# Performance work log

Measured on AMD Instinct MI355X. Metric: run time of the kernel, lower is better.

The kernel has to match this reference:

```python
import jax, jax.numpy as jnp
import numpy as np

PATCH = 8
EPS = 1e-5

def patch_split(x, s):
    # B C H W -> B s*s rH rW C
    B, C, H, W = x.shape
    rH, rW = H // s, W // s
    out = x.reshape(B, C, s, rH, s, rW)
    out = out.transpose(0, 2, 4, 3, 5, 1)
    return out.reshape(B, s * s, rH, rW, C)

def patch_recover(x, s):
    # B s*s rH rW C -> B C H W
    B, N, rH, rW, C = x.shape
    out = x.reshape(B, s, s, rH, rW, C)
    out = out.transpose(0, 5, 1, 3, 2, 4)
    return out.reshape(B, C, s * rH, s * rW)

def conv2d(x, w, pad):
    return jax.lax.conv_general_dilated(x, w, (1, 1), [(pad, pad), (pad, pad)],
                                        dimension_numbers=('NCHW', 'OIHW', 'NCHW'))

def bn_relu(x, g, b):
    # eval-mode BatchNorm2d with fresh running stats (mean=0, var=1)
    scale = (g / jnp.sqrt(1.0 + EPS))[None, :, None, None]
    return jax.nn.relu(x * scale + b[None, :, None, None])


def setup_inputs() -> dict:
    key = jax.random.key(0)
    ks = jax.random.split(key, 24)
    r = lambda i, shape, s=0.02: jax.random.normal(ks[i], shape, jnp.float32) * s
    B, H, W, C, K, P = 4, 64, 64, 512, 19, 64
    return {
        'M_1': jax.random.normal(ks[0], (B, 2048, H, W), jnp.float32),
        'F': jax.random.normal(ks[1], (B, C, H, W), jnp.float32),
        'I': jax.random.normal(ks[2], (B, K, H, W), jnp.float32),
        'R': jax.random.uniform(ks[3], (B, K, PATCH, PATCH), jnp.float32),
        'lg_w1': r(4, (P, P)), 'lg_w2': r(5, (C, C)),
        'fuse_w': r(6, (P,)), 'fuse_b': r(7, (1,)),
        'q_w': r(8, (256, C)), 'q_b': r(9, (256,)),
        'k_w': r(10, (256, C)), 'k_b': r(11, (256,)),
        'v_w': r(12, (256, C)), 'v_b': r(13, (256,)),
        'c1_w': r(14, (512, 256, 1, 1)),
        'bn1_g': jnp.ones((512,)), 'bn1_b': jnp.zeros((512,)),
        'c2_w': r(15, (512, 512, 3, 3)),
        'bn2_g': jnp.ones((512,)), 'bn2_b': jnp.zeros((512,)),
        'c3_w': r(16, (512, 2560, 3, 3)),
        'bn3_g': jnp.ones((512,)), 'bn3_b': jnp.zeros((512,)),
        'drop_w': r(17, (K, 512, 1, 1)),
    }


def reference(M_1, F, I, R, lg_w1, lg_w2, fuse_w, fuse_b, q_w, q_b, k_w, k_b,
              v_w, v_b, c1_w, bn1_g, bn1_b, c2_w, bn2_g, bn2_b, c3_w, bn3_g,
              bn3_b, drop_w):
    B = F.shape[0]
    F_p5 = patch_split(F, PATCH)          # B P rH rW C
    _, P, rH, rW, C = F_p5.shape
    I_p5 = patch_split(I, PATCH)          # B P rH rW K
    K = I_p5.shape[-1]
    F_p = F_p5.reshape(B, P, rH * rW, C)
    I_p = I_p5.reshape(B, P, rH * rW, K)
    bin_conf = R.reshape(B, K, P).transpose(0, 2, 1)[..., None]  # B P K 1
    pix = jax.nn.softmax(I_p, axis=2)
    F_l = jnp.einsum('bpnk,bpnc->bpkc', pix, F_p) * bin_conf     # B P K C
    # LG block: 1x1 conv over P channels, residual relu, linear over C
    h = jnp.einsum('qp,bpkc->bqkc', lg_w1, F_l)
    h = jax.nn.relu(h + F_l)
    F_l = jnp.einsum('bpkc,dc->bpkd', h, lg_w2)
    # FUSE: 1x1 conv P->1 (with bias); broadcast replaces torch .repeat
    F_g = jnp.einsum('p,bpkc->bkc', fuse_w, F_l) + fuse_b        # B K C
    query = jnp.einsum('bpnc,dc->bpnd', F_p, q_w) + q_b          # B P N 256
    key_ = jnp.einsum('bpkc,dc->bpkd', F_l, k_w) + k_b           # B P K 256
    value = jnp.einsum('bkc,dc->bkd', F_g, v_w) + v_b            # B K 256
    aff = jax.nn.softmax(jnp.einsum('bpnd,bpkd->bpnk', query, key_), axis=-1)
    F_s = jnp.einsum('bpnk,bkd->bpnd', aff, value)               # B P N 256
    F_s = patch_recover(F_s.reshape(B, P, rH, rW, -1), PATCH)    # B 256 H W
    Fo1 = F + bn_relu(conv2d(F_s, c1_w, 0), bn1_g, bn1_b)
    x2 = bn_relu(conv2d(Fo1, c2_w, 1), bn2_g, bn2_b)
    x3 = bn_relu(conv2d(jnp.concatenate([x2, M_1], axis=1), c3_w, 1), bn3_g, bn3_b)
    # Dropout2d is identity in eval; final 1x1 classifier conv
    return conv2d(x3, drop_w, 0)
```

## Files before the change

kernel.cpp:

```cpp
#include <hip/hip_runtime.h>
#include <hip/hip_bf16.h>

typedef __hip_bfloat16 bf16;
using short8 = __attribute__((ext_vector_type(8))) short;
using f32x4  = __attribute__((ext_vector_type(4))) float;

__device__ __forceinline__ float b2f(bf16 v){ return __bfloat162float(v); }
__device__ __forceinline__ bf16  f2b(float v){ return __float2bfloat16(v); }

#define EPSV 1e-5f

__device__ __forceinline__ void gload16(const void* g, void* l) {
  __builtin_amdgcn_global_load_lds(
      (const __attribute__((address_space(1))) unsigned int*)g,
      (__attribute__((address_space(3))) unsigned int*)l, 16, 0, 0);
}

__global__ __launch_bounds__(256) void k_cast4(
    const float* __restrict__ a, bf16* __restrict__ ao,
    const float* __restrict__ b, bf16* __restrict__ bo,
    const float* __restrict__ c, bf16* __restrict__ co,
    const float* __restrict__ d, bf16* __restrict__ dd) {
  int i = blockIdx.x * 256 + threadIdx.x;
  const float* src; bf16* dst; int off;
  if (i < 32768)       { src = a; dst = ao; off = i; }
  else if (i < 65536)  { src = b; dst = bo; off = i - 32768; }
  else if (i < 131072) { src = c; dst = co; off = i - 65536; }
  else                 { src = d; dst = dd; off = i - 131072; }
  float4 v = ((const float4*)src)[off];
  union { ushort4 u; bf16 h[4]; } o;
  o.h[0] = f2b(v.x); o.h[1] = f2b(v.y); o.h[2] = f2b(v.z); o.h[3] = f2b(v.w);
  ((ushort4*)dst)[off] = o.u;
}

__global__ __launch_bounds__(256) void k_wtr2(
    const float* __restrict__ wa, bf16* __restrict__ wta,
    const float* __restrict__ wb, bf16* __restrict__ wtb) {
  int oc = blockIdx.x, yy = blockIdx.y;
  const float* w; bf16* wt; int CI, c0;
  if (yy < 4) { w = wa; wt = wta; CI = 512;  c0 = yy * 128; }
  else        { w = wb; wt = wtb; CI = 2560; c0 = (yy - 4) * 128; }
  __shared__ float ld[128 * 9];
  const float* src = w + ((size_t)oc * CI + c0) * 9;
  for (int i = threadIdx.x; i < 128 * 9; i += 256) ld[i] = src[i];
  __syncthreads();
  for (int i = threadIdx.x; i < 128 * 9; i += 256) {
    int k9 = i / 128, t = i - k9 * 128;
    wt[((size_t)k9 * 512 + oc) * CI + c0 + t] = f2b(ld[t * 9 + k9]);
  }
}

__global__ __launch_bounds__(256) void k_m1t(const float* __restrict__ M1,
                                             bf16* __restrict__ M1b) {
  int b = blockIdx.x >> 6, y = blockIdx.x & 63;
  int c0 = blockIdx.y * 64;
  __shared__ float t[64][65];
  for (int i = threadIdx.x; i < 4096; i += 256) {
    int cc = i >> 6, x = i & 63;
    t[x][cc] = M1[((size_t)(b * 2048 + c0 + cc) * 64 + y) * 64 + x];
  }
  __syncthreads();
  for (int i = threadIdx.x; i < 4096; i += 256) {
    int x = i >> 6, cc = i & 63;
    M1b[((size_t)((b * 64 + y) * 64 + x)) * 2048 + c0 + cc] = f2b(t[x][cc]);
  }
}

__global__ __launch_bounds__(256) void k_fp2(const float* __restrict__ F,
                                             bf16* __restrict__ FP) {
  int b = blockIdx.x >> 6, y = blockIdx.x & 63;
  int tid = threadIdx.x;
  __shared__ float t[256][65];
  int p_hi = (y >> 3) << 3, n_hi = (y & 7) << 3;
  for (int half = 0; half < 2; half++) {
    int c0 = half << 8;
    for (int i = tid; i < 256 * 64; i += 256) {
      int cc = i >> 6, x = i & 63;
      t[cc][x] = F[((size_t)(b * 512 + c0 + cc) * 64 + y) * 64 + x];
    }
    __syncthreads();
    for (int x = 0; x < 64; x++) {
      int p = p_hi + (x >> 3), n = n_hi + (x & 7);
      FP[((size_t)(b * 64 + p)) * 32768 + n * 512 + c0 + tid] = f2b(t[tid][x]);
    }
    __syncthreads();
  }
}

__global__ __launch_bounds__(256) void k_flocal2(const float* __restrict__ I,
        const float* __restrict__ R, const bf16* __restrict__ FP,
        float* __restrict__ FL0) {
  int bp = blockIdx.x, b = bp >> 6, p = bp & 63;
  int tid = threadIdx.x, w = tid >> 6, lane = tid & 63;
  __shared__ __align__(16) bf16 fps[64 * 512];
  __shared__ float pix[19][64];
  __shared__ float bc[19];
  {
    const bf16* src = FP + (size_t)bp * 32768 + lane * 8;
    #pragma unroll
    for (int t = 0; t < 16; t++) {
      int chunk = w + t * 4;
      gload16(src + chunk * 512, (char*)fps + chunk * 1024);
    }
  }
  int py = (p >> 3) * 8, px = (p & 7) * 8;
  for (int i = tid; i < 19 * 64; i += 256) {
    int k = i >> 6, n = i & 63;
    int y = py + (n >> 3), x = px + (n & 7);
    pix[k][n] = I[((size_t)(b * 19 + k) * 64 + y) * 64 + x];
  }
  if (tid < 19) bc[tid] = R[(size_t)(b * 19 + tid) * 64 + p];
  __syncthreads();
  if (tid < 19) {
    float mx = -1e30f;
    for (int n = 0; n < 64; n++) mx = fmaxf(mx, pix[tid][n]);
    float s = 0.f;
    for (int n = 0; n < 64; n++) { float e = __expf(pix[tid][n] - mx); pix[tid][n] = e; s += e; }
    float sc = bc[tid] / s;
    for (int n = 0; n < 64; n++) pix[tid][n] *= sc;
  }
  __syncthreads();
  for (int task = tid; task < 19 * 64; task += 256) {
    int k = task >> 6, c8 = (task & 63) << 3;
    float acc[8] = {};
    for (int n = 0; n < 64; n++) {
      float pv = pix[k][n];
      union { short8 s; bf16 h[8]; } v;
      v.s = *(const short8*)&fps[n * 512 + c8];
      #pragma unroll
      for (int j = 0; j < 8; j++) acc[j] += pv * b2f(v.h[j]);
    }
    float* dst = FL0 + ((size_t)(b * 64 + p) * 19 + k) * 512 + c8;
    #pragma unroll
    for (int j = 0; j < 8; j++) dst[j] = acc[j];
  }
}

__global__ __launch_bounds__(256) void k_lg1(const float* __restrict__ FL0,
        const float* __restrict__ w1, bf16* __restrict__ Hb) {
  int tid = threadIdx.x;
  int b = blockIdx.y;
  int n0 = blockIdx.x * 256;
  __shared__ float W[64][64];
  __shared__ float Xs[16][256];
  for (int i = tid; i < 4096; i += 256) W[i >> 6][i & 63] = w1[i];
  float acc[64];
  #pragma unroll
  for (int po = 0; po < 64; po++) acc[po] = 0.f;
  for (int q0 = 0; q0 < 64; q0 += 16) {
    __syncthreads();
    for (int i = tid; i < 4096; i += 256) {
      int q = i >> 8, j = i & 255;
      Xs[q][j] = FL0[(size_t)(b * 64 + q0 + q) * 9728 + n0 + j];
    }
    __syncthreads();
    for (int q = 0; q < 16; q++) {
      float xv = Xs[q][tid];
      #pragma unroll
      for (int po = 0; po < 64; po++) acc[po] += W[po][q0 + q] * xv;
    }
  }
  for (int po = 0; po < 64; po++) {
    float r = acc[po] + FL0[(size_t)(b * 64 + po) * 9728 + n0 + tid];
    Hb[(size_t)(b * 64 + po) * 9728 + n0 + tid] = f2b(fmaxf(r, 0.f));
  }
}

template<int MODE>
__global__ __launch_bounds__(256) void k_gmm(
    const bf16* __restrict__ A, const bf16* __restrict__ B,
    const float* __restrict__ bias, float* __restrict__ C,
    bf16* __restrict__ Cb, int N, int K,
    const float* __restrict__ g, const float* __restrict__ bb,
    const float* __restrict__ Fres, bf16* __restrict__ outb) {
  int tid = threadIdx.x;
  int m0 = blockIdx.x * 128, n0 = blockIdx.y * 128;
  int w = tid >> 6, lane = tid & 63, ln = lane & 15, qd = lane >> 4;
  int wm = w & 1, wn = w >> 1;
  __shared__ __align__(16) char smem[34816];

  f32x4 acc[4][4];
  #pragma unroll
  for (int i = 0; i < 4; i++)
    #pragma unroll
    for (int j = 0; j < 4; j++) acc[i][j] = (f32x4){0.f, 0.f, 0.f, 0.f};

  int rsub = lane >> 2, ch = lane & 3;
  auto stage = [&](int p) {
    char* base = smem + (p & 1) * 16384;
    int k0 = p << 5;
    #pragma unroll
    for (int t = 0; t < 2; t++) {
      int ii = w + t * 4;
      int r = ii * 16 + rsub;
      int sw = (ch ^ ((r >> 1) & 3)) << 3;
      gload16(A + (size_t)(m0 + r) * K + k0 + sw, base + ii * 1024);
      gload16(B + (size_t)(n0 + r) * K + k0 + sw, base + 8192 + ii * 1024);
    }
  };
  auto compute = [&](int p) {
    const char* base = smem + (p & 1) * 16384;
    short8 af[4], bv[4];
    #pragma unroll
    for (int mi = 0; mi < 4; mi++) {
      int r = wm * 64 + mi * 16 + ln;
      af[mi] = *(const short8*)(base + r * 64 + ((qd ^ ((r >> 1) & 3)) << 4));
    }
    #pragma unroll
    for (int ni = 0; ni < 4; ni++) {
      int r = wn * 64 + ni * 16 + ln;
      bv[ni] = *(const short8*)(base + 8192 + r * 64 + ((qd ^ ((r >> 1) & 3)) << 4));
    }
    #pragma unroll
    for (int mi = 0; mi < 4; mi++)
      #pragma unroll
      for (int ni = 0; ni < 4; ni++)
        acc[mi][ni] = __builtin_amdgcn_mfma_f32_16x16x32_bf16(
            af[mi], bv[ni], acc[mi][ni], 0, 0, 0);
  };

  int KT = K >> 5;
  stage(0);
  __syncthreads();
  for (int p = 0; p < KT; p++) {
    if (p + 1 < KT) stage(p + 1);
    compute(p);
    __syncthreads();
  }

  if (MODE <= 1) {
    #pragma unroll
    for (int mi = 0; mi < 4; mi++) {
      #pragma unroll
      for (int r = 0; r < 4; r++) {
        int m = m0 + wm * 64 + mi * 16 + qd * 4 + r;
        #pragma unroll
        for (int ni = 0; ni < 4; ni++) {
          int n = n0 + wn * 64 + ni * 16 + ln;
          float v = acc[mi][ni][r];
          if (bias) v += bias[n];
          C[(size_t)m * N + n] = v;
          if (MODE == 1) Cb[(size_t)m * N + n] = f2b(v);
        }
      }
    }
  } else {
    bf16* EP = (bf16*)smem;
    int b = n0 >> 12;
    #pragma unroll
    for (int mi = 0; mi < 4; mi++) {
      #pragma unroll
      for (int r = 0; r < 4; r++) {
        int ml = wm * 64 + mi * 16 + qd * 4 + r;
        int oc = m0 + ml;
        float sc = g[oc] * rsqrtf(1.f + EPSV);
        float bt = bb[oc];
        #pragma unroll
        for (int ni = 0; ni < 4; ni++) {
          int nl = wn * 64 + ni * 16 + ln;
          int pix = n0 + nl;
          int y = (pix >> 6) & 63, x = pix & 63;
          float v = fmaxf(acc[mi][ni][r] * sc + bt, 0.f)
                  + Fres[((size_t)(b * 512 + oc) * 64 + y) * 64 + x];
          EP[nl * 136 + ml] = f2b(v);
        }
      }
    }
    __syncthreads();
    int pl = tid >> 1, half = tid & 1;
    size_t gb = (size_t)(n0 + pl) * 512 + m0 + half * 64;
    const bf16* row = &EP[pl * 136 + half * 64];
    #pragma unroll
    for (int j2 = 0; j2 < 8; j2++)
      *(short8*)(outb + gb + j2 * 8) = *(const short8*)(row + j2 * 8);
  }
}

__global__ __launch_bounds__(256) void k_fusev(const float* __restrict__ FL,
        const float* __restrict__ fw, const float* __restrict__ fbv,
        const float* __restrict__ vw, const float* __restrict__ vb,
        float* __restrict__ VAL) {
  int tid = threadIdx.x;
  int bk = blockIdx.x, b = bk / 19, k = bk % 19;
  __shared__ float fwl[64];
  __shared__ __align__(16) float fg[512];
  if (tid < 64) fwl[tid] = fw[tid];
  __syncthreads();
  float fbias = fbv[0];
  for (int c = tid; c < 512; c += 256) {
    float s = 0.f;
    for (int p = 0; p < 64; p++)
      s += fwl[p] * FL[((size_t)(b * 64 + p) * 19 + k) * 512 + c];
    fg[c] = s + fbias;
  }
  __syncthreads();
  int d = tid;
  float s = vb[d];
  const float4* vr = (const float4*)(vw + (size_t)d * 512);
  const float4* fr = (const float4*)fg;
  for (int c4 = 0; c4 < 128; c4++) {
    float4 wv = vr[c4], f = fr[c4];
    s += f.x * wv.x + f.y * wv.y + f.z * wv.z + f.w * wv.w;
  }
  VAL[(size_t)bk * 256 + d] = s;
}

__global__ __launch_bounds__(256) void k_attn(const float* __restrict__ Q,
        const float* __restrict__ KEY, const float* __restrict__ VAL,
        bf16* __restrict__ FS) {
  int tid = threadIdx.x;
  int bp = blockIdx.x, b = bp >> 6, p = bp & 63;
  __shared__ __align__(16) float ks[19][256];
  __shared__ __align__(16) float vs[19][256];
  __shared__ float Ss[64][20];
  __shared__ bf16 ot[64][256];
  for (int i = tid; i < 19 * 256; i += 256) {
    ks[i >> 8][i & 255] = KEY[(size_t)bp * 19 * 256 + i];
    vs[i >> 8][i & 255] = VAL[(size_t)b * 19 * 256 + i];
  }
  __syncthreads();
  {
    int n = tid >> 2, kq = tid & 3;
    const float4* qrow = (const float4*)(Q + ((size_t)bp * 64 + n) * 256);
    for (int k = kq; k < 19; k += 4) {
      const float4* kr = (const float4*)&ks[k][0];
      float s = 0.f;
      for (int d4 = 0; d4 < 64; d4++) {
        float4 qv = qrow[d4], kv = kr[d4];
        s += qv.x * kv.x + qv.y * kv.y + qv.z * kv.z + qv.w * kv.w;
      }
      Ss[n][k] = s;
    }
  }
  __syncthreads();
  if (tid < 64) {
    float mx = -1e30f;
    for (int k = 0; k < 19; k++) mx = fmaxf(mx, Ss[tid][k]);
    float sum = 0.f;
    for (int k = 0; k < 19; k++) { float e = __expf(Ss[tid][k] - mx); Ss[tid][k] = e; sum += e; }
    float inv = 1.f / sum;
    for (int k = 0; k < 19; k++) Ss[tid][k] *= inv;
  }
  __syncthreads();
  {
    int d = tid;
    for (int nn = 0; nn < 64; nn++) {
      float s = 0.f;
      #pragma unroll
      for (int k = 0; k < 19; k++) s += Ss[nn][k] * vs[k][d];
      ot[nn][d] = f2b(s);
    }
  }
  __syncthreads();
  {
    int py = (p >> 3) * 8, px = (p & 7) * 8;
    int nn = tid >> 2, q = tid & 3;
    int y = py + (nn >> 3), x = px + (nn & 7);
    size_t gb = (((size_t)(b * 64 + y) * 64) + x) * 256 + q * 64;
    const bf16* row = &ot[nn][q * 64];
    #pragma unroll
    for (int j = 0; j < 8; j++)
      *(short8*)(FS + gb + j * 8) = *(const short8*)(row + j * 8);
  }
}

__global__ __launch_bounds__(512) void k_conv3(
    const bf16* __restrict__ Xin, int Cin,
    const bf16* __restrict__ M1b, const float* __restrict__ M1f, int C2,
    const bf16* __restrict__ WT,
    const float* __restrict__ g, const float* __restrict__ bb,
    bf16* __restrict__ out, int Cos) {
  int tid = threadIdx.x;
  int b = blockIdx.x >> 4, y0 = (blockIdx.x & 15) * 4;
  int oc0 = blockIdx.y * 128;
  int w = tid >> 6, lane = tid & 63, ln = lane & 15, qd = lane >> 4;
  int wocg = w & 1, wyp = w >> 1;
  int Ct = Cin + C2;

  __shared__ __align__(16) char smem[125440];
  char* smA  = smem;
  char* smB  = smem + 73728;
  char* dump = smem + 124416;

  for (int bufi = 0; bufi < 2; bufi++) {
    char* bbuf = smB + bufi * 25344;
    for (int i = tid; i < 6 * 2 * 32; i += 512) {
      int rl = i >> 6, hh = (i >> 5) & 1, kk = i & 31;
      *(bf16*)(bbuf + (rl * 66 + (hh ? 65 : 0)) * 64 + kk * 2) = f2b(0.f);
    }
    if (y0 == 0)
      for (int i = tid; i < 66 * 16; i += 512) ((float*)bbuf)[i] = 0.f;
    if (y0 == 60)
      for (int i = tid; i < 66 * 16; i += 512)
        ((float*)(bbuf + 5 * 66 * 64))[i] = 0.f;
  }

  f32x4 acc[4][4];
  #pragma unroll
  for (int i = 0; i < 4; i++)
    #pragma unroll
    for (int j = 0; j < 4; j++) acc[i][j] = (f32x4){0.f, 0.f, 0.f, 0.f};

  int ngroups = Ct >> 5;
  int NPH = ngroups * 3;

  auto stageA = [&](int p) {
    int c0 = (p / 3) << 5, ky = p % 3;
    char* base = smA + (p % 3 == p - (p / 3) * 3 ? 0 : 0) ;
    base = smA + (p % 3) * 0;
    base = smA + ((p % 3) == 0 ? 0 : 0);
    base = smA + ky * 0;
    base = smA + (p % 3) * 24576;
    #pragma unroll
    for (int t = 0; t < 3; t++) {
      int j = w + t * 8;
      int kx = j >> 3, i8 = j & 7;
      int ocl = i8 * 16 + (lane >> 2);
      const bf16* src = WT + ((size_t)((ky * 3 + kx) * 512 + oc0 + ocl) * Ct + c0)
                      + (((lane & 3) ^ ((ocl >> 1) & 3)) << 3);
      gload16(src, base + (kx * 128 + i8 * 16) * 64);
    }
  };
  auto stageB = [&](int gi) {
    int c0 = gi << 5;
    char* bbuf = smB + (gi & 1) * 25344;
    if (c0 < Cin || M1b != nullptr) {
      const bf16* T; int Cs, cb;
      if (c0 < Cin) { T = Xin; Cs = Cin; cb = c0; }
      else          { T = M1b; Cs = C2;  cb = c0 - Cin; }
      #pragma unroll
      for (int t = 0; t < 3; t++) {
        int j = w + t * 8;
        int rl = j >> 2, q = j & 3;
        int yy = y0 + rl - 1;
        bool ok = (unsigned)yy < 64u;
        int yc = ok ? yy : y0;
        int xx = q * 16 + (lane >> 2), xr = xx + 1;
        const bf16* src = T + ((size_t)((b * 64 + yc) * 64 + xx) * Cs + cb)
                        + (((lane & 3) ^ ((xr >> 1) & 3)) << 3);
        char* dst = ok ? (bbuf + (rl * 66 + 1 + q * 16) * 64) : dump;
        gload16(src, dst);
      }
    } else {
      if (w < 6) {
        int rl = w, yy = y0 + rl - 1;
        if ((unsigned)yy < 64u) {
          int xx = lane, xr = xx + 1;
          const float* mp = M1f + ((size_t)(b * 2048 + (c0 - Cin)) * 64 + yy) * 64 + xx;
          #pragma unroll
          for (int q = 0; q < 8; q++) {
            union { ushort4 u; bf16 h[4]; } pk;
            #pragma unroll
            for (int jj = 0; jj < 4; jj++) pk.h[jj] = f2b(mp[(size_t)(q * 4 + jj) * 4096]);
            *(ushort4*)(bbuf + (rl * 66 + xr) * 64
                        + ((((q >> 1) ^ ((xr >> 1) & 3)) << 4) | ((q & 1) << 3))) = pk.u;
          }
        }
      }
      asm volatile("s_waitcnt lgkmcnt(0)" ::: "memory");
    }
  };
  auto computeP = [&](int p) {
    int ky = p % 3;
    const char* base = smA + (p % 3) * 24576;
    const char* bB   = smB + ((p / 3) & 1) * 25344;
    int rl = wyp + ky;
    #pragma unroll
    for (int kx = 0; kx < 3; kx++) {
      short8 af[4], bv[4];
      #pragma unroll
      for (int mi = 0; mi < 4; mi++) {
        int ocl = wocg * 64 + mi * 16 + ln;
        af[mi] = *(const short8*)(base + (kx * 128 + ocl) * 64
                                  + ((qd ^ ((ocl >> 1) & 3)) << 4));
      }
      #pragma unroll
      for (int ni = 0; ni < 4; ni++) {
        int xr = ni * 16 + ln + kx;
        bv[ni] = *(const short8*)(bB + (rl * 66 + xr) * 64
                                  + ((qd ^ ((xr >> 1) & 3)) << 4));
      }
      #pragma unroll
      for (int mi = 0; mi < 4; mi++)
        #pragma unroll
        for (int ni = 0; ni < 4; ni++)
          acc[mi][ni] = __builtin_amdgcn_mfma_f32_16x16x32_bf16(
              af[mi], bv[ni], acc[mi][ni], 0, 0, 0);
    }
  };

  stageB(0);
  stageA(0);
  stageA(1);
  asm volatile("s_waitcnt lgkmcnt(0)" ::: "memory");

  for (int p = 0; p < NPH; p++) {
    __builtin_amdgcn_s_barrier();
    __builtin_amdgcn_sched_barrier(0);
    if (p + 2 < NPH) stageA(p + 2);
    int pm3 = p % 3;
    int gn = p / 3 + 1;
    bool bValid = gn < ngroups;
    bool bFastN = bValid && (((gn << 5) < Cin) || (M1b != nullptr));
    if (pm3 == 1 && bValid) stageB(gn);
    __builtin_amdgcn_sched_barrier(0);
    int N = (p + 1 < NPH ? 3 : 0) + (p + 2 < NPH ? 3 : 0)
          + ((pm3 != 0 && bFastN) ? 3 : 0);
    if (N == 9)      asm volatile("s_waitcnt vmcnt(9)" ::: "memory");
    else if (N == 6) asm volatile("s_waitcnt vmcnt(6)" ::: "memory");
    else if (N == 3) asm volatile("s_waitcnt vmcnt(3)" ::: "memory");
    else             asm volatile("s_waitcnt vmcnt(0)" ::: "memory");
    __builtin_amdgcn_sched_barrier(0);
    __builtin_amdgcn_s_setprio(1);
    computeP(p);
    __builtin_amdgcn_s_setprio(0);
  }
  __syncthreads();

  {
    bf16* EP = (bf16*)smem;
    #pragma unroll
    for (int mi = 0; mi < 4; mi++) {
      int oclb = wocg * 64 + mi * 16 + qd * 4;
      float sc[4], bt[4];
      #pragma unroll
      for (int r = 0; r < 4; r++) {
        int oc = oc0 + oclb + r;
        sc[r] = g[oc] * rsqrtf(1.f + EPSV);
        bt[r] = bb[oc];
      }
      #pragma unroll
      for (int ni = 0; ni < 4; ni++) {
        int x = ni * 16 + ln;
        union { ushort4 u; bf16 h[4]; } pk;
        #pragma unroll
        for (int r = 0; r < 4; r++)
          pk.h[r] = f2b(fmaxf(acc[mi][ni][r] * sc[r] + bt[r], 0.f));
        *(ushort4*)&EP[(wyp * 64 + x) * 128 + oclb] = pk.u;
      }
    }
    __syncthreads();
    int pixl = tid >> 1, hh = tid & 1;
    int yloc = pixl >> 6, x = pixl & 63;
    size_t gb = ((size_t)((b * 64 + y0 + yloc) * 64 + x)) * Cos + oc0 + hh * 64;
    const bf16* row = &EP[pixl * 128 + hh * 64];
    #pragma unroll
    for (int k = 0; k < 8; k++)
      *(short8*)(out + gb + k * 8) = *(const short8*)(row + k * 8);
  }
}

__global__ __launch_bounds__(256) void k_final(const bf16* __restrict__ X3,
        const float* __restrict__ dw, float* __restrict__ out) {
  int tid = threadIdx.x;
  int b = blockIdx.x >> 6, y = blockIdx.x & 63;
  __shared__ float W[19 * 512];
  for (int i = tid; i < 19 * 512; i += 256) W[i] = dw[i];
  __syncthreads();
  int x = tid & 63, kg = tid >> 6;
  const bf16* px = X3 + (((size_t)(b * 64 + y) * 64) + x) * 512;
  float acc[5] = {0.f, 0.f, 0.f, 0.f, 0.f};
  for (int c8 = 0; c8 < 512; c8 += 8) {
    union { short8 s; bf16 h[8]; } v;
    v.s = *(const short8*)(px + c8);
    float f[8];
    #pragma unroll
    for (int j = 0; j < 8; j++) f[j] = b2f(v.h[j]);
    #pragma unroll
    for (int i = 0; i < 5; i++) {
      int k = kg * 5 + i;
      if (k < 19) {
        const float* wr = &W[k * 512 + c8];
        #pragma unroll
        for (int j = 0; j < 8; j++) acc[i] += f[j] * wr[j];
      }
    }
  }
  for (int i = 0; i < 5; i++) {
    int k = kg * 5 + i;
    if (k < 19) out[((size_t)(b * 19 + k) * 64 + y) * 64 + x] = acc[i];
  }
}

extern "C" void kernel_launch(void* const* d_in, const int* in_sizes, int n_in,
                              void* d_out, int out_size, void* d_ws, size_t ws_size,
                              hipStream_t stream) {
  (void)in_sizes; (void)n_in; (void)out_size;
  const float* M1 = (const float*)d_in[0];
  const float* F  = (const float*)d_in[1];
  const float* Iin= (const float*)d_in[2];
  const float* R  = (const float*)d_in[3];
  const float* w1 = (const float*)d_in[4];
  const float* w2 = (const float*)d_in[5];
  const float* fw = (const float*)d_in[6];
  const float* fb = (const float*)d_in[7];
  const float* qw = (const float*)d_in[8];
  const float* qb = (const float*)d_in[9];
  const float* kw = (const float*)d_in[10];
  const float* kb = (const float*)d_in[11];
  const float* vw = (const float*)d_in[12];
  const float* vb = (const float*)d_in[13];
  const float* c1 = (const float*)d_in[14];
  const float* g1 = (const float*)d_in[15];
  const float* b1 = (const float*)d_in[16];
  const float* c2 = (const float*)d_in[17];
  const float* g2 = (const float*)d_in[18];
  const float* b2 = (const float*)d_in[19];
  const float* c3 = (const float*)d_in[20];
  const float* g3 = (const float*)d_in[21];
  const float* b3 = (const float*)d_in[22];
  const float* dw = (const float*)d_in[23];

  char* ws = (char*)d_ws;
  bool fast = ws_size >= (size_t)137363456ULL;

  bf16*  qwb  = (bf16*)(ws + 0);
  bf16*  kwb  = (bf16*)(ws + 262144);
  bf16*  w2b  = (bf16*)(ws + 524288);
  bf16*  c1b  = (bf16*)(ws + 1048576);
  bf16*  WT2  = (bf16*)(ws + 0);
  bf16*  WT3  = (bf16*)(ws + 4718592);
  bf16*  FS   = (bf16*)(ws + 28311552);
  bf16*  FO1  = (bf16*)(ws + 36700160);
  bf16*  X2   = (bf16*)(ws + 53477376);
  bf16*  M1bf = fast ? (bf16*)(ws + 70254592) : nullptr;
  bf16*  X3   = (bf16*)(ws + 28311552);
  bf16*  FP    = (bf16*) (ws + 53477376);
  float* QUERY = (float*)(ws + 70254592);
  float* FL0   = (float*)(ws + 87031808);
  bf16*  Hb    = (bf16*) (ws + 96993280);
  bf16*  FLb   = (bf16*) (ws + 101974016);
  float* KEY   = (float*)(ws + 106954752);
  float* VAL   = (float*)(ws + 111935488);
  float* FL    = FL0;

  k_cast4<<<640, 256, 0, stream>>>(qw, qwb, kw, kwb, w2, w2b, c1, c1b);
  k_fp2<<<256, 256, 0, stream>>>(F, FP);
  k_flocal2<<<256, 256, 0, stream>>>(Iin, R, FP, FL0);
  k_lg1<<<dim3(38, 4), 256, 0, stream>>>(FL0, w1, Hb);
  k_gmm<1><<<dim3(38, 4), 256, 0, stream>>>(Hb, w2b, nullptr, FL, FLb, 512, 512,
                                            nullptr, nullptr, nullptr, nullptr);
  k_fusev<<<76, 256, 0, stream>>>(FL, fw, fb, vw, vb, VAL);
  k_gmm<0><<<dim3(38, 2), 256, 0, stream>>>(FLb, kwb, kb, KEY, nullptr, 256, 512,
                                            nullptr, nullptr, nullptr, nullptr);
  k_gmm<0><<<dim3(128, 2), 256, 0, stream>>>(FP, qwb, qb, QUERY, nullptr, 256, 512,
                                             nullptr, nullptr, nullptr, nullptr);
  k_attn<<<256, 256, 0, stream>>>(QUERY, KEY, VAL, FS);
  if (fast) k_m1t<<<dim3(256, 32), 256, 0, stream>>>(M1, M1bf);
  k_gmm<2><<<dim3(4, 128), 256, 0, stream>>>(c1b, FS, nullptr, nullptr, nullptr,
                                             16384, 256, g1, b1, F, FO1);
  k_wtr2<<<dim3(512, 24), 256, 0, stream>>>(c2, WT2, c3, WT3);
  k_conv3<<<dim3(64, 4), 512, 0, stream>>>(FO1, 512, nullptr, nullptr, 0,
                                           WT2, g2, b2, X2, 512);
  k_conv3<<<dim3(64, 4), 512, 0, stream>>>(X2, 512, M1bf, M1, 2048,
                                           WT3, g3, b3, X3, 512);
  k_final<<<256, 256, 0, stream>>>(X3, dw, (float*)d_out);
}
```

Baseline: 972.0 us.

## Load conv3 weights directly into registers instead of staging through LDS

Removes the LDS staging buffer for the weight (A) operand of the 3x3 conv over the concatenated input. Each lane now loads its own MFMA A fragments from global memory into registers and double-buffers them across ky phases, while only the input tile (B) stays in shared memory. This cuts LDS use from about 125KB to about 66KB, which could allow more blocks per CU, and drops the LDS traffic for A. In exchange it adds many register-held fragments and uncoalesced 16-byte global loads whose latency is no longer hidden by the explicit vmcnt pipelining, and several waves re-read the same weights from global memory.

```diff
diff --git a/kernel.cpp b/kernel.cpp
--- a/kernel.cpp
+++ b/kernel.cpp
@@ -377,10 +377,9 @@
   int wocg = w & 1, wyp = w >> 1;
   int Ct = Cin + C2;
 
-  __shared__ __align__(16) char smem[125440];
-  char* smA  = smem;
-  char* smB  = smem + 73728;
-  char* dump = smem + 124416;
+  __shared__ __align__(16) char smem[66560];
+  char* smB  = smem;
+  char* dump = smem + 65536;
 
   for (int bufi = 0; bufi < 2; bufi++) {
     char* bbuf = smB + bufi * 25344;
@@ -402,25 +401,9 @@
     for (int j = 0; j < 4; j++) acc[i][j] = (f32x4){0.f, 0.f, 0.f, 0.f};
 
   int ngroups = Ct >> 5;
-  int NPH = ngroups * 3;
-
-  auto stageA = [&](int p) {
-    int c0 = (p / 3) << 5, ky = p % 3;
-    char* base = smA + (p % 3 == p - (p / 3) * 3 ? 0 : 0) ;
-    base = smA + (p % 3) * 0;
-    base = smA + ((p % 3) == 0 ? 0 : 0);
-    base = smA + ky * 0;
-    base = smA + (p % 3) * 24576;
-    #pragma unroll
-    for (int t = 0; t < 3; t++) {
-      int j = w + t * 8;
-      int kx = j >> 3, i8 = j & 7;
-      int ocl = i8 * 16 + (lane >> 2);
-      const bf16* src = WT + ((size_t)((ky * 3 + kx) * 512 + oc0 + ocl) * Ct + c0)
-                      + (((lane & 3) ^ ((ocl >> 1) & 3)) << 3);
-      gload16(src, base + (kx * 128 + i8 * 16) * 64);
-    }
-  };
+
+  const bf16* Alane = WT + (size_t)(oc0 + wocg * 64 + ln) * Ct + qd * 8;
+
   auto stageB = [&](int gi) {
     int c0 = gi << 5;
     char* bbuf = smB + (gi & 1) * 25344;
@@ -457,23 +440,22 @@
           }
         }
       }
-      asm volatile("s_waitcnt lgkmcnt(0)" ::: "memory");
     }
   };
-  auto computeP = [&](int p) {
-    int ky = p % 3;
-    const char* base = smA + (p % 3) * 24576;
-    const char* bB   = smB + ((p / 3) & 1) * 25344;
+  auto loadA = [&](short8* dst, int ky, int c0) {
+    #pragma unroll
+    for (int kx = 0; kx < 3; kx++)
+      #pragma unroll
+      for (int mi = 0; mi < 4; mi++)
+        dst[kx * 4 + mi] = *(const short8*)(Alane
+            + (size_t)((ky * 3 + kx) * 512 + mi * 16) * Ct + c0);
+  };
+  auto computeP = [&](const short8* A, int ky, int gpar) {
+    const char* bB = smB + gpar * 25344;
     int rl = wyp + ky;
     #pragma unroll
     for (int kx = 0; kx < 3; kx++) {
-      short8 af[4], bv[4];
-      #pragma unroll
-      for (int mi = 0; mi < 4; mi++) {
-        int ocl = wocg * 64 + mi * 16 + ln;
-        af[mi] = *(const short8*)(base + (kx * 128 + ocl) * 64
-                                  + ((qd ^ ((ocl >> 1) & 3)) << 4));
-      }
+      short8 bv[4];
       #pragma unroll
       for (int ni = 0; ni < 4; ni++) {
         int xr = ni * 16 + ln + kx;
@@ -485,37 +467,37 @@
         #pragma unroll
         for (int ni = 0; ni < 4; ni++)
           acc[mi][ni] = __builtin_amdgcn_mfma_f32_16x16x32_bf16(
-              af[mi], bv[ni], acc[mi][ni], 0, 0, 0);
+              A[kx * 4 + mi], bv[ni], acc[mi][ni], 0, 0, 0);
     }
   };
 
+  short8 Aa[12], Ab[12];
   stageB(0);
-  stageA(0);
-  stageA(1);
-  asm volatile("s_waitcnt lgkmcnt(0)" ::: "memory");
-
-  for (int p = 0; p < NPH; p++) {
-    __builtin_amdgcn_s_barrier();
-    __builtin_amdgcn_sched_barrier(0);
-    if (p + 2 < NPH) stageA(p + 2);
-    int pm3 = p % 3;
-    int gn = p / 3 + 1;
-    bool bValid = gn < ngroups;
-    bool bFastN = bValid && (((gn << 5) < Cin) || (M1b != nullptr));
-    if (pm3 == 1 && bValid) stageB(gn);
-    __builtin_amdgcn_sched_barrier(0);
-    int N = (p + 1 < NPH ? 3 : 0) + (p + 2 < NPH ? 3 : 0)
-          + ((pm3 != 0 && bFastN) ? 3 : 0);
-    if (N == 9)      asm volatile("s_waitcnt vmcnt(9)" ::: "memory");
-    else if (N == 6) asm volatile("s_waitcnt vmcnt(6)" ::: "memory");
-    else if (N == 3) asm volatile("s_waitcnt vmcnt(3)" ::: "memory");
-    else             asm volatile("s_waitcnt vmcnt(0)" ::: "memory");
-    __builtin_amdgcn_sched_barrier(0);
-    __builtin_amdgcn_s_setprio(1);
-    computeP(p);
-    __builtin_amdgcn_s_setprio(0);
-  }
-  __syncthreads();
+  loadA(Aa, 0, 0);
+  __syncthreads();
+
+  for (int gi = 0; gi < ngroups; gi += 2) {
+    int c0 = gi << 5, c1 = c0 + 32, c2 = c0 + 64;
+    bool hb1 = gi + 1 < ngroups;
+    bool hb2 = gi + 2 < ngroups;
+    loadA(Ab, 1, c0);
+    computeP(Aa, 0, 0);
+    loadA(Aa, 2, c0);
+    if (hb1) stageB(gi + 1);
+    computeP(Ab, 1, 0);
+    if (hb1) loadA(Ab, 0, c1);
+    computeP(Aa, 2, 0);
+    __syncthreads();
+    if (!hb1) break;
+    loadA(Aa, 1, c1);
+    computeP(Ab, 0, 1);
+    loadA(Ab, 2, c1);
+    if (hb2) stageB(gi + 2);
+    computeP(Aa, 1, 1);
+    if (hb2) loadA(Aa, 0, c2);
+    computeP(Ab, 2, 1);
+    __syncthreads();
+  }
 
   {
     bf16* EP = (bf16*)smem;
```

New measurement: 3.425 ms. 3.52x slower.
